# Kernel optimization log

Hardware: AMD Instinct MI355X
Metric: run time of the kernel (lower is better)

Reference implementation:

```python
import jax, jax.numpy as jnp
import numpy as np

B, N_PER_GRAPH = 16, 512          # uniform graphs -> to_dense_batch is a reshape
N_TOKENS = B * N_PER_GRAPH
M = 32                            # neighbors per node
D_MODEL, D_EDGE, H = 256, 128, 8


def _layernorm(x, g, b, eps=1e-5):
    m = jnp.mean(x, axis=-1, keepdims=True)
    v = jnp.mean((x - m) ** 2, axis=-1, keepdims=True)
    return (x - m) * jax.lax.rsqrt(v + eps) * g + b


def _frame_ops():
    # 2^3 = 8 sign-flip operations, matches FrameAveraging.create_ops
    d = jnp.array([-1.0, 1.0], dtype=jnp.float32)
    g = jnp.meshgrid(d, d, d, indexing='ij')
    return jnp.stack(g, axis=-1).reshape(8, 3)


def _forward(token_embs, geo_feats, edge_feats, neighbor_indices, neighbor_masks,
             ln_qkv_g, ln_qkv_b, W_qkv, b_qkv, ln_e_g, ln_e_b, W_qkv_e, b_qkv_e,
             w_attn, w_edge, W_gate, b_gate, W_fc1, b_fc1, ln_h_g, ln_h_b,
             W_fc2, b_fc2, W_fa, b_fa):
    n = token_embs.shape[0]
    d_head = D_MODEL // H
    de_head = D_EDGE // H
    # qkv transformation
    qkv = _layernorm(token_embs, ln_qkv_g, ln_qkv_b) @ W_qkv + b_qkv
    q, k, v = [a.reshape(n, H, d_head) for a in jnp.split(qkv, 3, axis=-1)]
    qkve = _layernorm(edge_feats, ln_e_g, ln_e_b) @ W_qkv_e + b_qkv_e
    qe, ve = [a.reshape(n, M, H, de_head) for a in jnp.split(qkve, 2, axis=-1)]
    gate = jax.nn.sigmoid(token_embs @ W_gate + b_gate)            # [n,1]
    # GAT-style MLP attention over gathered neighbors
    message = q[:, None] + k[neighbor_indices]                     # [n,M,H,d]
    attn = jnp.einsum('nmhd,d->nmh', message, w_attn) \
         + jnp.einsum('nmhe,e->nmh', qe, w_edge)
    attn = jnp.where(neighbor_masks[..., None], attn, -1e9)
    attn = jax.nn.softmax(jnp.transpose(attn, (0, 2, 1)), axis=-1)  # [n,H,M]
    # context aggregation
    v_n = v[neighbor_indices]                                      # [n,M,H,d]
    scalar_ctx = jnp.einsum('nhm,nmhd->nhd', attn, v_n).reshape(n, -1)
    edge_ctx = jnp.einsum('nhm,nmhd->nhd', attn, ve).reshape(n, -1)
    hcat = jnp.concatenate([scalar_ctx, edge_ctx], axis=-1)
    hmid = _layernorm(jax.nn.gelu(hcat @ W_fc1 + b_fc1, approximate=False), ln_h_g, ln_h_b)
    scalar_out = hmid @ W_fc2 + b_fc2 + token_embs
    # geometric branch with frame averaging (n_heads > 1 path)
    Xb = geo_feats.reshape(B, N_PER_GRAPH, 3)                      # dense batch, full mask
    center = Xb.mean(axis=1)                                       # [B,3]
    Xc = Xb - center[:, None]
    C = jax.lax.stop_gradient(jnp.einsum('bni,bnj->bij', Xc, Xc))  # backward=False -> detach
    _, V = jnp.linalg.eigh(C)                                      # symmetric, UPLO irrelevant
    ops = _frame_ops()
    F_ops = jax.lax.stop_gradient(ops[None, :, None, :] * V[:, None])  # [B,8,3,3]
    h_fr = jnp.einsum('bpj,boji->bopi', Xc, F_ops)                 # [B,8,N,3]
    geo_f = jnp.transpose(h_fr, (1, 0, 2, 3)).reshape(8, n, 3)     # frame-major, node order b*N+p
    geo_neigh = geo_f[:, neighbor_indices]                         # [8,n,M,3]
    geo_ctx = jnp.einsum('nhm,fnmd->fnhd', attn, geo_neigh)        # [8,n,H,3]
    agg = jax.nn.silu(jnp.einsum('fnhd,h->fnd', geo_ctx, W_fa) + b_fa)  # W_frame_agg
    geo_b = jnp.transpose(agg, (1, 0, 2)).reshape(B, N_PER_GRAPH, 8, 3)
    geo_b = jnp.transpose(geo_b, (0, 2, 1, 3))                     # [B,8,N,3]
    inv = jnp.einsum('boij,bopj->bopi', F_ops, geo_b).mean(axis=1) + center[:, None]
    geo_context = inv.reshape(n, 3)
    geo_out = geo_context * gate + geo_feats * (1.0 - gate)
    return scalar_out, geo_out


def setup_inputs() -> dict:
    key = jax.random.key(0)
    ks = jax.random.split(key, 16)
    r = lambda k, shape, s=0.02: (jax.random.normal(k, shape) * s).astype(jnp.float32)
    token_embs = jax.random.normal(ks[0], (N_TOKENS, D_MODEL), dtype=jnp.float32)
    geo_feats = jax.random.normal(ks[1], (N_TOKENS, 3), dtype=jnp.float32)
    edge_feats = jax.random.normal(ks[2], (N_TOKENS, M, D_EDGE), dtype=jnp.float32)
    base = (jnp.arange(N_TOKENS) // N_PER_GRAPH) * N_PER_GRAPH
    neighbor_indices = base[:, None] + jax.random.randint(ks[3], (N_TOKENS, M), 0, N_PER_GRAPH)
    batch_idx = jnp.arange(N_TOKENS) // N_PER_GRAPH
    neighbor_masks = jax.random.uniform(ks[4], (N_TOKENS, M)) < 0.9
    d_head, de_head = D_MODEL // H, D_EDGE // H
    return dict(
        token_embs=token_embs, geo_feats=geo_feats, edge_feats=edge_feats,
        neighbor_indices=neighbor_indices, batch_idx=batch_idx, neighbor_masks=neighbor_masks,
        ln_qkv_g=jnp.ones(D_MODEL), ln_qkv_b=jnp.zeros(D_MODEL),
        W_qkv=r(ks[5], (D_MODEL, 3 * D_MODEL)), b_qkv=jnp.zeros(3 * D_MODEL),
        ln_e_g=jnp.ones(D_EDGE), ln_e_b=jnp.zeros(D_EDGE),
        W_qkv_e=r(ks[6], (D_EDGE, 2 * D_EDGE)), b_qkv_e=jnp.zeros(2 * D_EDGE),
        w_attn=r(ks[7], (d_head,), 0.1), w_edge=r(ks[8], (de_head,), 0.1),
        W_gate=jnp.zeros((D_MODEL, 1)), b_gate=jnp.ones((1,)),   # _init_params
        W_fc1=r(ks[9], (D_MODEL + D_EDGE, D_MODEL)), b_fc1=jnp.zeros(D_MODEL),
        ln_h_g=jnp.ones(D_MODEL), ln_h_b=jnp.zeros(D_MODEL),
        W_fc2=r(ks[10], (D_MODEL, D_MODEL)), b_fc2=jnp.zeros(D_MODEL),
        W_fa=r(ks[11], (H,), 0.3), b_fa=jnp.zeros((1,)),
    )


def reference(token_embs, geo_feats, edge_feats, neighbor_indices, batch_idx, neighbor_masks,
              ln_qkv_g, ln_qkv_b, W_qkv, b_qkv, ln_e_g, ln_e_b, W_qkv_e, b_qkv_e,
              w_attn, w_edge, W_gate, b_gate, W_fc1, b_fc1, ln_h_g, ln_h_b,
              W_fc2, b_fc2, W_fa, b_fa):
    # batch_idx is uniform (arange // N_PER_GRAPH); dense batching handled by reshape
    return _forward(token_embs, geo_feats, edge_feats, neighbor_indices, neighbor_masks,
                    ln_qkv_g, ln_qkv_b, W_qkv, b_qkv, ln_e_g, ln_e_b, W_qkv_e, b_qkv_e,
                    w_attn, w_edge, W_gate, b_gate, W_fc1, b_fc1, ln_h_g, ln_h_b,
                    W_fc2, b_fc2, W_fa, b_fa)
```

## Files before the change

kernel.cpp:

```cpp
#include <hip/hip_runtime.h>
#include <math.h>

#define NTOK 8192
#define NPG  512
#define MNEI 32
#define DM   256
#define DE   128
#define NH   8

#define OFF_WV    0u
#define OFF_WQAK  65536u
#define OFF_BCAT  69632u
#define OFF_WEF   69904u
#define OFF_BEF   70928u
#define OFF_FLAG  70936u
#define OFF_QA    70944u
#define OFF_KA    136480u
#define OFF_GATE  202016u
#define OFF_VW    210208u
#define OFF_PROJ  2307360u
#define OFF_VMAT  2331936u
#define OFF_CEN   2332080u
#define OFF_HCAT  2332128u

#define OUT_GEO_OFF 2097152

__device__ __forceinline__ void fma4x4(const float4 a, const float4 w, float4* acc) {
    acc[0].x += a.x*w.x; acc[0].y += a.x*w.y; acc[0].z += a.x*w.z; acc[0].w += a.x*w.w;
    acc[1].x += a.y*w.x; acc[1].y += a.y*w.y; acc[1].z += a.y*w.z; acc[1].w += a.y*w.w;
    acc[2].x += a.z*w.x; acc[2].y += a.z*w.y; acc[2].z += a.z*w.z; acc[2].w += a.z*w.w;
    acc[3].x += a.w*w.x; acc[3].y += a.w*w.y; acc[3].z += a.w*w.z; acc[3].w += a.w*w.w;
}

__device__ __forceinline__ float dot4(const float4 a, const float4 b) {
    return a.x*b.x + a.y*b.y + a.z*b.z + a.w*b.w;
}

__global__ __launch_bounds__(256) void k_fold(
    const float* __restrict__ Wqkv, const float* __restrict__ bqkv,
    const float* __restrict__ Wqkve, const float* __restrict__ bqkve,
    const float* __restrict__ w_attn, const float* __restrict__ w_edge,
    const int* __restrict__ maskp, float* __restrict__ ws)
{
    int t = threadIdx.x;
    if (blockIdx.x == 0) {
        __shared__ int sbad, sflt;
        if (t == 0) { sbad = 0; sflt = 0; }
        __syncthreads();
        int bad = 0, flt = 0;
        for (int i = 0; i < 256; i++) {
            unsigned int w = (unsigned int)maskp[i*256 + t];
            if (w > 1u) bad = 1;
            if (w == 0x3F800000u) flt = 1;
        }
        if (bad) atomicOr(&sbad, 1);
        if (flt) atomicOr(&sflt, 1);
        __syncthreads();
        if (t == 0) {
            int f = sflt ? 2 : (sbad ? 1 : 0);
            ((int*)(ws + OFF_FLAG))[0] = f;
        }
        return;
    }
    int gid = (blockIdx.x - 1) * 256 + t;
    if (gid < 65536) {
        int k = gid >> 8, c = gid & 255;
        ws[OFF_WV + gid] = Wqkv[k*768 + 512 + c];
    } else if (gid < 69632) {
        int idx = gid - 65536;
        int c = idx >> 8, k = idx & 255;
        int h = c & 7; int off = (c < 8) ? 0 : 256;
        float s = 0.f;
        for (int d = 0; d < 32; d++) s += Wqkv[k*768 + off + h*32 + d] * w_attn[d];
        ws[OFF_WQAK + idx] = s;
    } else if (gid < 69632 + 272) {
        int c = gid - 69632;
        float val;
        if (c < 16) {
            int h = c & 7; int off = (c < 8) ? 0 : 256;
            float s = 0.f;
            for (int d = 0; d < 32; d++) s += bqkv[off + h*32 + d] * w_attn[d];
            val = s;
        } else {
            val = bqkv[512 + (c - 16)];
        }
        ws[OFF_BCAT + c] = val;
    } else if (gid < 69904 + 1024) {
        int i = gid - 69904;
        int h = i >> 7, r = i & 127;
        float s = 0.f;
        for (int e = 0; e < 16; e++) s += Wqkve[r*256 + h*16 + e] * w_edge[e];
        ws[OFF_WEF + i] = s;
    } else if (gid < 70928 + 8) {
        int h = gid - 70928;
        float s = 0.f;
        for (int e = 0; e < 16; e++) s += bqkve[h*16 + e] * w_edge[e];
        ws[OFF_BEF + h] = s;
    }
}

__global__ __launch_bounds__(256) void k_tokprep(
    const float* __restrict__ tok, const float* __restrict__ ln_g,
    const float* __restrict__ ln_b, const float* __restrict__ Wgate,
    const float* __restrict__ bgate, float* __restrict__ ws)
{
    __shared__ __align__(16) float sln[256 * 12];
    int t = threadIdx.x;
    int tok0 = blockIdx.x * 8;

    #pragma unroll
    for (int q = 0; q < 8; q++)
        sln[t*12 + q] = tok[(size_t)(tok0 + q) * 256 + t];
    __syncthreads();

    int wave = t >> 6, lane = t & 63;
    for (int rr = 0; rr < 2; rr++) {
        int tt = wave * 2 + rr;
        float s = 0.f, gdot = 0.f;
        float xs[4];
        #pragma unroll
        for (int q = 0; q < 4; q++) {
            int k = lane + 64*q;
            float x = sln[k*12 + tt];
            xs[q] = x; s += x; gdot += x * Wgate[k];
        }
        for (int m = 32; m >= 1; m >>= 1) { s += __shfl_xor(s,m,64); gdot += __shfl_xor(gdot,m,64); }
        float mu = s * (1.0f/256.0f);
        float vs = 0.f;
        #pragma unroll
        for (int q = 0; q < 4; q++) { float d = xs[q]-mu; vs += d*d; }
        for (int m = 32; m >= 1; m >>= 1) vs += __shfl_xor(vs,m,64);
        float rinv = rsqrtf(vs*(1.0f/256.0f)+1e-5f);
        #pragma unroll
        for (int q = 0; q < 4; q++) {
            int k = lane + 64*q;
            sln[k*12 + tt] = (xs[q]-mu)*rinv*ln_g[k] + ln_b[k];
        }
        if (lane == 0) ws[OFF_GATE + tok0 + tt] = 1.0f/(1.0f+expf(-(gdot + bgate[0])));
    }
    __syncthreads();

    if (t < 128) {
        int i = t >> 6, j = t & 63;
        const float* Wc = ws + OFF_WV + 4*j;
        float4 acc[4];
        acc[0] = acc[1] = acc[2] = acc[3] = make_float4(0.f,0.f,0.f,0.f);
        #pragma unroll 8
        for (int k = 0; k < 256; k++) {
            float4 a4 = *(const float4*)&sln[k*12 + 4*i];
            float4 w4 = *(const float4*)&Wc[(size_t)k*256];
            fma4x4(a4, w4, acc);
        }
        float4 b4 = *(const float4*)&ws[OFF_BCAT + 16 + 4*j];
        #pragma unroll
        for (int ti = 0; ti < 4; ti++) {
            int n = tok0 + 4*i + ti;
            float4 v = acc[ti];
            v.x += b4.x; v.y += b4.y; v.z += b4.z; v.w += b4.w;
            *(float4*)&ws[OFF_VW + (size_t)n*256 + 4*j] = v;
        }
    } else {
        int wave3 = (t >> 6) - 2;
        int col = t & 15, tp = (t & 63) >> 4;
        int tokn = wave3*4 + tp;
        const float* wq = ws + OFF_WQAK + col*256;
        float acc = 0.f;
        #pragma unroll 8
        for (int k4 = 0; k4 < 64; k4++) {
            float4 w4 = *(const float4*)&wq[4*k4];
            acc += w4.x * sln[(4*k4+0)*12 + tokn]
                 + w4.y * sln[(4*k4+1)*12 + tokn]
                 + w4.z * sln[(4*k4+2)*12 + tokn]
                 + w4.w * sln[(4*k4+3)*12 + tokn];
        }
        acc += ws[OFF_BCAT + col];
        int n = tok0 + tokn;
        if (col < 8) ws[OFF_QA + n*8 + col] = acc;
        else         ws[OFF_KA + n*8 + (col - 8)] = acc;
    }
}

__global__ __launch_bounds__(256) void k_geo(const float* __restrict__ geo, float* __restrict__ ws)
{
    __shared__ float sred[4 * 9];
    __shared__ float sres[9];
    __shared__ float sV[9];
    int t = threadIdx.x, g = blockIdx.x;
    int wave = t >> 6, lane = t & 63;
    const float* gp = geo + (size_t)g * NPG * 3;

    float x0[2], y0[2], z0[2];
    float sx = 0.f, sy = 0.f, sz = 0.f;
    for (int i = 0; i < 2; i++) {
        int p = t + 256 * i;
        x0[i] = gp[p*3 + 0]; y0[i] = gp[p*3 + 1]; z0[i] = gp[p*3 + 2];
        sx += x0[i]; sy += y0[i]; sz += z0[i];
    }
    {
        float vals[3] = {sx, sy, sz};
        for (int q = 0; q < 3; q++) {
            float v = vals[q];
            for (int m = 32; m >= 1; m >>= 1) v += __shfl_xor(v, m, 64);
            if (lane == 0) sred[wave*9 + q] = v;
        }
    }
    __syncthreads();
    if (t < 3) {
        float s = 0.f;
        for (int w = 0; w < 4; w++) s += sred[w*9 + t];
        sres[t] = s * (1.0f / 512.0f);
    }
    __syncthreads();
    float cx = sres[0], cy = sres[1], cz = sres[2];

    float c6[6] = {0.f, 0.f, 0.f, 0.f, 0.f, 0.f};
    for (int i = 0; i < 2; i++) {
        float dx = x0[i] - cx, dy = y0[i] - cy, dz = z0[i] - cz;
        c6[0] += dx*dx; c6[1] += dx*dy; c6[2] += dx*dz;
        c6[3] += dy*dy; c6[4] += dy*dz; c6[5] += dz*dz;
    }
    for (int q = 0; q < 6; q++) {
        float v = c6[q];
        for (int m = 32; m >= 1; m >>= 1) v += __shfl_xor(v, m, 64);
        if (lane == 0) sred[wave*9 + q] = v;
    }
    __syncthreads();
    if (t < 6) {
        float s = 0.f;
        for (int w = 0; w < 4; w++) s += sred[w*9 + t];
        sres[t] = s;
    }
    __syncthreads();

    if (t == 0) {
        double a[3][3];
        a[0][0] = sres[0]; a[0][1] = a[1][0] = sres[1]; a[0][2] = a[2][0] = sres[2];
        a[1][1] = sres[3]; a[1][2] = a[2][1] = sres[4]; a[2][2] = sres[5];
        double v[3][3] = {{1,0,0},{0,1,0},{0,0,1}};
        const int ps[3] = {0, 0, 1}, qs[3] = {1, 2, 2};
        for (int sweep = 0; sweep < 10; sweep++) {
            for (int pi = 0; pi < 3; pi++) {
                int p = ps[pi], q = qs[pi];
                double apq = a[p][q];
                if (fabs(apq) < 1e-300) continue;
                double theta = (a[q][q] - a[p][p]) / (2.0 * apq);
                double tt = ((theta >= 0.0) ? 1.0 : -1.0) / (fabs(theta) + sqrt(theta*theta + 1.0));
                double c = 1.0 / sqrt(tt*tt + 1.0), s = tt * c;
                int k = 3 - p - q;
                double app = a[p][p], aqq = a[q][q], akp = a[k][p], akq = a[k][q];
                a[p][p] = app - tt * apq;
                a[q][q] = aqq + tt * apq;
                a[p][q] = 0.0; a[q][p] = 0.0;
                a[k][p] = c*akp - s*akq; a[p][k] = a[k][p];
                a[k][q] = s*akp + c*akq; a[q][k] = a[k][q];
                for (int kk = 0; kk < 3; kk++) {
                    double vp = v[kk][p], vq = v[kk][q];
                    v[kk][p] = c*vp - s*vq;
                    v[kk][q] = s*vp + c*vq;
                }
            }
        }
        for (int r = 0; r < 3; r++)
            for (int c2 = 0; c2 < 3; c2++) {
                float fv = (float)v[r][c2];
                sV[r*3 + c2] = fv;
                ws[OFF_VMAT + g*9 + r*3 + c2] = fv;
            }
        ws[OFF_CEN + g*3 + 0] = cx;
        ws[OFF_CEN + g*3 + 1] = cy;
        ws[OFF_CEN + g*3 + 2] = cz;
    }
    __syncthreads();

    for (int i = 0; i < 2; i++) {
        int p = t + 256 * i;
        float dx = x0[i] - cx, dy = y0[i] - cy, dz = z0[i] - cz;
        for (int c = 0; c < 3; c++) {
            float pr = dx * sV[0*3 + c] + dy * sV[1*3 + c] + dz * sV[2*3 + c];
            ws[OFF_PROJ + (size_t)(g*NPG + p)*3 + c] = pr;
        }
    }
}

__global__ __launch_bounds__(256) void k_attn(
    const float* __restrict__ edge, const int* __restrict__ nbr,
    const void* __restrict__ maskp,
    const float* __restrict__ lneg, const float* __restrict__ lneb,
    const float* __restrict__ bqkve, const float* __restrict__ Wqkve,
    const float* __restrict__ Wfa, const float* __restrict__ bfa,
    const float* __restrict__ geo, float* __restrict__ ws, float* __restrict__ out)
{
    __shared__ __align__(16) float se[32 * 132];
    __shared__ __align__(16) float uSWE[8 * 132];
    __shared__ __align__(16) float sew[8 * 132];
    __shared__ __align__(16) float sattn[8 * 36];
    __shared__ int   snbr[32];
    __shared__ int   smask[32];
    __shared__ float sqa[8], sbef[8];
    __shared__ float sg3[4];

    int t = threadIdx.x;
    int n = blockIdx.x;
    int g = n >> 9;
    int flag = ((const int*)(ws + OFF_FLAG))[0];

    if (t < 32) {
        snbr[t] = nbr[n*32 + t];
        int mv;
        if (flag == 1)      mv = (int)((const unsigned char*)maskp)[n*32 + t];
        else if (flag == 2) mv = (((const float*)maskp)[n*32 + t] != 0.0f) ? 1 : 0;
        else                mv = ((const int*)maskp)[n*32 + t];
        smask[t] = mv;
    }
    if (t < 8) { sqa[t] = ws[OFF_QA + n*8 + t]; sbef[t] = ws[OFF_BEF + t]; }
    {
        int idx = t * 4;
        int h = idx >> 7, r = idx & 127;
        int sub = r >> 4, c = r & 15;
        *(float4*)&uSWE[sub*132 + h*16 + c] = *(const float4*)&ws[OFF_WEF + idx];
    }
    {
        const float4* ep = (const float4*)(edge + (size_t)n * 4096);
        #pragma unroll
        for (int j = 0; j < 4; j++) {
            int l = j*1024 + t*4;
            float4 v4 = ep[l >> 2];
            int m = l >> 7, r = l & 127;
            *(float4*)&se[m*132 + r] = v4;
        }
    }
    __syncthreads();

    int m = t >> 3, sub = t & 7;
    {
        int base = m*132 + sub*16;
        float4 x0 = *(float4*)&se[base + 0];
        float4 x1 = *(float4*)&se[base + 4];
        float4 x2 = *(float4*)&se[base + 8];
        float4 x3 = *(float4*)&se[base + 12];
        float s = x0.x+x0.y+x0.z+x0.w + x1.x+x1.y+x1.z+x1.w
                + x2.x+x2.y+x2.z+x2.w + x3.x+x3.y+x3.z+x3.w;
        for (int mm = 4; mm >= 1; mm >>= 1) s += __shfl_xor(s, mm, 8);
        float mu = s * (1.0f / 128.0f);
        float vs = (x0.x-mu)*(x0.x-mu) + (x0.y-mu)*(x0.y-mu) + (x0.z-mu)*(x0.z-mu) + (x0.w-mu)*(x0.w-mu)
                 + (x1.x-mu)*(x1.x-mu) + (x1.y-mu)*(x1.y-mu) + (x1.z-mu)*(x1.z-mu) + (x1.w-mu)*(x1.w-mu)
                 + (x2.x-mu)*(x2.x-mu) + (x2.y-mu)*(x2.y-mu) + (x2.z-mu)*(x2.z-mu) + (x2.w-mu)*(x2.w-mu)
                 + (x3.x-mu)*(x3.x-mu) + (x3.y-mu)*(x3.y-mu) + (x3.z-mu)*(x3.z-mu) + (x3.w-mu)*(x3.w-mu);
        for (int mm = 4; mm >= 1; mm >>= 1) vs += __shfl_xor(vs, mm, 8);
        float rinv = rsqrtf(vs * (1.0f / 128.0f) + 1e-5f);
        const float4* gp4 = (const float4*)(lneg + sub*16);
        const float4* bp4 = (const float4*)(lneb + sub*16);
        float4 g0 = gp4[0], g1 = gp4[1], g2 = gp4[2], g3 = gp4[3];
        float4 b0 = bp4[0], b1 = bp4[1], b2 = bp4[2], b3 = bp4[3];
        x0.x=(x0.x-mu)*rinv*g0.x+b0.x; x0.y=(x0.y-mu)*rinv*g0.y+b0.y;
        x0.z=(x0.z-mu)*rinv*g0.z+b0.z; x0.w=(x0.w-mu)*rinv*g0.w+b0.w;
        x1.x=(x1.x-mu)*rinv*g1.x+b1.x; x1.y=(x1.y-mu)*rinv*g1.y+b1.y;
        x1.z=(x1.z-mu)*rinv*g1.z+b1.z; x1.w=(x1.w-mu)*rinv*g1.w+b1.w;
        x2.x=(x2.x-mu)*rinv*g2.x+b2.x; x2.y=(x2.y-mu)*rinv*g2.y+b2.y;
        x2.z=(x2.z-mu)*rinv*g2.z+b2.z; x2.w=(x2.w-mu)*rinv*g2.w+b2.w;
        x3.x=(x3.x-mu)*rinv*g3.x+b3.x; x3.y=(x3.y-mu)*rinv*g3.y+b3.y;
        x3.z=(x3.z-mu)*rinv*g3.z+b3.z; x3.w=(x3.w-mu)*rinv*g3.w+b3.w;
        *(float4*)&se[base + 0]  = x0;
        *(float4*)&se[base + 4]  = x1;
        *(float4*)&se[base + 8]  = x2;
        *(float4*)&se[base + 12] = x3;

        float accl[8];
        const float* wb = &uSWE[sub*132];
        #pragma unroll
        for (int h = 0; h < 8; h++) {
            const float4* wp = (const float4*)(wb + h*16);
            accl[h] = dot4(x0,wp[0]) + dot4(x1,wp[1]) + dot4(x2,wp[2]) + dot4(x3,wp[3]);
        }
        #pragma unroll
        for (int st = 1; st < 8; st <<= 1) {
            #pragma unroll
            for (int h = 0; h < 8; h++) accl[h] += __shfl_xor(accl[h], st, 8);
        }
        float myacc = accl[0];
        #pragma unroll
        for (int h = 1; h < 8; h++) myacc = (sub == h) ? accl[h] : myacc;
        float lg = sqa[sub] + sbef[sub] + myacc + ws[OFF_KA + snbr[m]*8 + sub];
        if (!smask[m]) lg = -1e9f;
        sattn[sub*36 + m] = lg;
    }
    __syncthreads();

    {
        int h = t >> 5, m2 = t & 31;
        float x = sattn[h*36 + m2];
        float mx = x;
        for (int mm = 16; mm >= 1; mm >>= 1) mx = fmaxf(mx, __shfl_xor(mx, mm, 32));
        float e = expf(x - mx);
        float sum = e;
        for (int mm = 16; mm >= 1; mm >>= 1) sum += __shfl_xor(sum, mm, 32);
        sattn[h*36 + m2] = e / sum;
    }
    __syncthreads();

    float* sq = uSWE;

    float4 accS = make_float4(0.f,0.f,0.f,0.f);
    if (t < 128) {
        int half = t >> 6, c4 = t & 63;
        int h = c4 >> 3;
        const float* vw = ws + OFF_VW;
        #pragma unroll 4
        for (int mi = 0; mi < 16; mi++) {
            int mm2 = half*16 + mi;
            float a = sattn[h*36 + mm2];
            int row = snbr[mm2];
            float4 v4 = *(const float4*)&vw[(size_t)row*256 + 4*c4];
            accS.x += a*v4.x; accS.y += a*v4.y; accS.z += a*v4.z; accS.w += a*v4.w;
        }
        if (half) *(float4*)&sq[c4*4] = accS;
        if (t < 32) {
            float wmv = 0.f;
            #pragma unroll
            for (int h2 = 0; h2 < 8; h2++) wmv += Wfa[h2] * sattn[h2*36 + t];
            int row = snbr[t];
            const float* pp = ws + OFF_PROJ + (size_t)row*3;
            float q0 = wmv * pp[0], q1 = wmv * pp[1], q2 = wmv * pp[2];
            for (int st = 16; st >= 1; st >>= 1) {
                q0 += __shfl_xor(q0, st, 32);
                q1 += __shfl_xor(q1, st, 32);
                q2 += __shfl_xor(q2, st, 32);
            }
            if (t < 3) {
                float sd = (t == 0) ? q0 : (t == 1) ? q1 : q2;
                float bb = bfa[0];
                float p1 = sd + bb, p2 = -sd + bb;
                float s1v = p1 / (1.0f + expf(-p1));
                float s2v = p2 / (1.0f + expf(-p2));
                sg3[t] = 0.5f * (s1v - s2v);
            }
        }
    } else {
        int rq = t & 31, hb = (t >> 5) - 4;
        float4 e1 = make_float4(0.f,0.f,0.f,0.f);
        float4 e2 = make_float4(0.f,0.f,0.f,0.f);
        #pragma unroll
        for (int mq = 0; mq < 8; mq++) {
            float4 a4a = *(const float4*)&sattn[hb*36 + 4*mq];
            float4 a4b = *(const float4*)&sattn[(hb+4)*36 + 4*mq];
            float aa[4] = {a4a.x, a4a.y, a4a.z, a4a.w};
            float ab[4] = {a4b.x, a4b.y, a4b.z, a4b.w};
            #pragma unroll
            for (int c = 0; c < 4; c++) {
                int mm2 = 4*mq + c;
                float4 e4 = *(const float4*)&se[mm2*132 + rq*4];
                e1.x += aa[c]*e4.x; e1.y += aa[c]*e4.y; e1.z += aa[c]*e4.z; e1.w += aa[c]*e4.w;
                e2.x += ab[c]*e4.x; e2.y += ab[c]*e4.y; e2.z += ab[c]*e4.z; e2.w += ab[c]*e4.w;
            }
        }
        *(float4*)&sew[hb*132 + rq*4]     = e1;
        *(float4*)&sew[(hb+4)*132 + rq*4] = e2;
    }
    __syncthreads();

    float* sec = se;
    float4 accE = make_float4(0.f,0.f,0.f,0.f);
    {
        int col4 = t & 31, rgrp = t >> 5;
        int h2 = col4 >> 2;
        const float* wqb = Wqkve + 128 + 4*col4;
        #pragma unroll 4
        for (int ri = 0; ri < 16; ri++) {
            int r = rgrp*16 + ri;
            float sv = sew[h2*132 + r];
            float4 w4 = *(const float4*)&wqb[(size_t)r*256];
            accE.x += sv*w4.x; accE.y += sv*w4.y; accE.z += sv*w4.z; accE.w += sv*w4.w;
        }
        if (t < 64) {
            float4 p = *(const float4*)&sq[t*4];
            float4 tot;
            tot.x = accS.x + p.x; tot.y = accS.y + p.y;
            tot.z = accS.z + p.z; tot.w = accS.w + p.w;
            *(float4*)&ws[OFF_HCAT + (size_t)n*384 + 4*t] = tot;
        }
        *(float4*)&sec[rgrp*128 + col4*4] = accE;
    }
    __syncthreads();

    if (t < 128) {
        float ec = bqkve[128 + t];
        #pragma unroll
        for (int g2 = 0; g2 < 8; g2++) ec += sec[g2*128 + t];
        ws[OFF_HCAT + (size_t)n*384 + 256 + t] = ec;
    }
    if (t < 3) {
        const float* Vm = ws + OFF_VMAT + g*9;
        float gc = Vm[t*3+0]*sg3[0] + Vm[t*3+1]*sg3[1] + Vm[t*3+2]*sg3[2] + ws[OFF_CEN + g*3 + t];
        float gt = ws[OFF_GATE + n];
        out[OUT_GEO_OFF + (size_t)n*3 + t] = gc * gt + geo[(size_t)n*3 + t] * (1.0f - gt);
    }
}

__global__ __launch_bounds__(256) void k_mlp(
    const float* __restrict__ tok, const float* __restrict__ Wfc1,
    const float* __restrict__ bfc1, const float* __restrict__ lnhg,
    const float* __restrict__ lnhb, const float* __restrict__ Wfc2,
    const float* __restrict__ bfc2, const float* __restrict__ ws,
    float* __restrict__ out)
{
    __shared__ __align__(16) float A[384 * 12];
    __shared__ __align__(16) float R[128 * 16];
    int t = threadIdx.x;
    int tok0 = blockIdx.x * 8;
    int i2 = (t >> 6) & 1, kh = t >> 7, j = t & 63;
    const float* hc = ws + OFF_HCAT;

    #pragma unroll
    for (int q = 0; q < 12; q++) {
        int idx = q*256 + t;
        int tt = idx / 384;
        int k  = idx - tt*384;
        A[k*12 + tt] = hc[(size_t)tok0*384 + idx];
    }
    __syncthreads();

    float4 acc1[4];
    acc1[0] = acc1[1] = acc1[2] = acc1[3] = make_float4(0.f,0.f,0.f,0.f);
    {
        const float* wp = Wfc1 + 4*j;
        int kbase = kh * 192;
        #pragma unroll 8
        for (int kk = 0; kk < 192; kk++) {
            int k = kbase + kk;
            float4 a4 = *(const float4*)&A[k*12 + 4*i2];
            float4 w4 = *(const float4*)&wp[(size_t)k*256];
            fma4x4(a4, w4, acc1);
        }
    }
    if (kh == 1) {
        int rowid = t - 128;
        #pragma unroll
        for (int ti = 0; ti < 4; ti++) *(float4*)&R[rowid*16 + ti*4] = acc1[ti];
    }
    __syncthreads();

    float h[4][4];
    if (kh == 0) {
        float4 b4 = *(const float4*)&bfc1[4*j];
        #pragma unroll
        for (int ti = 0; ti < 4; ti++) {
            float4 p = *(const float4*)&R[t*16 + ti*4];
            float xv[4] = {acc1[ti].x + p.x + b4.x, acc1[ti].y + p.y + b4.y,
                           acc1[ti].z + p.z + b4.z, acc1[ti].w + p.w + b4.w};
            #pragma unroll
            for (int c = 0; c < 4; c++) {
                float x = xv[c];
                h[ti][c] = 0.5f * x * (1.0f + erff(x * 0.70710678118654752f));
            }
        }
        float s[4], qv[4];
        #pragma unroll
        for (int ti = 0; ti < 4; ti++) {
            s[ti]  = h[ti][0] + h[ti][1] + h[ti][2] + h[ti][3];
            qv[ti] = h[ti][0]*h[ti][0] + h[ti][1]*h[ti][1] + h[ti][2]*h[ti][2] + h[ti][3]*h[ti][3];
        }
        for (int m = 32; m >= 1; m >>= 1)
            #pragma unroll
            for (int ti = 0; ti < 4; ti++) {
                s[ti]  += __shfl_xor(s[ti], m, 64);
                qv[ti] += __shfl_xor(qv[ti], m, 64);
            }
        float4 g4 = *(const float4*)&lnhg[4*j];
        float4 b42 = *(const float4*)&lnhb[4*j];
        float gg[4] = {g4.x, g4.y, g4.z, g4.w};
        float bb[4] = {b42.x, b42.y, b42.z, b42.w};
        #pragma unroll
        for (int ti = 0; ti < 4; ti++) {
            float mu = s[ti] * (1.0f/256.0f);
            float var = qv[ti] * (1.0f/256.0f) - mu*mu;
            float rinv = rsqrtf(var + 1e-5f);
            #pragma unroll
            for (int c = 0; c < 4; c++) {
                float hn = (h[ti][c] - mu) * rinv * gg[c] + bb[c];
                A[(4*j + c)*12 + 4*i2 + ti] = hn;
            }
        }
    }
    __syncthreads();

    float4 acc2[4];
    acc2[0] = acc2[1] = acc2[2] = acc2[3] = make_float4(0.f,0.f,0.f,0.f);
    {
        const float* wp = Wfc2 + 4*j;
        int kbase = kh * 128;
        #pragma unroll 8
        for (int kk = 0; kk < 128; kk++) {
            int k = kbase + kk;
            float4 a4 = *(const float4*)&A[k*12 + 4*i2];
            float4 w4 = *(const float4*)&wp[(size_t)k*256];
            fma4x4(a4, w4, acc2);
        }
    }
    if (kh == 1) {
        int rowid = t - 128;
        #pragma unroll
        for (int ti = 0; ti < 4; ti++) *(float4*)&R[rowid*16 + ti*4] = acc2[ti];
    }
    __syncthreads();

    if (kh == 0) {
        float4 b4 = *(const float4*)&bfc2[4*j];
        #pragma unroll
        for (int ti = 0; ti < 4; ti++) {
            float4 p = *(const float4*)&R[t*16 + ti*4];
            size_t o = (size_t)(tok0 + 4*i2 + ti) * 256 + 4*j;
            float4 r4 = *(const float4*)&tok[o];
            float4 v;
            v.x = acc2[ti].x + p.x + b4.x + r4.x;
            v.y = acc2[ti].y + p.y + b4.y + r4.y;
            v.z = acc2[ti].z + p.z + b4.z + r4.z;
            v.w = acc2[ti].w + p.w + b4.w + r4.w;
            *(float4*)&out[o] = v;
        }
    }
}

extern "C" void kernel_launch(void* const* d_in, const int* in_sizes, int n_in,
                              void* d_out, int out_size, void* d_ws, size_t ws_size,
                              hipStream_t stream) {
    (void)in_sizes; (void)n_in; (void)out_size; (void)ws_size;
    const float* tok   = (const float*)d_in[0];
    const float* geo   = (const float*)d_in[1];
    const float* edge  = (const float*)d_in[2];
    const int*   nbr   = (const int*)d_in[3];
    const void*  maskp = d_in[5];
    const float* ln_qkv_g = (const float*)d_in[6];
    const float* ln_qkv_b = (const float*)d_in[7];
    const float* Wqkv  = (const float*)d_in[8];
    const float* bqkv  = (const float*)d_in[9];
    const float* ln_e_g = (const float*)d_in[10];
    const float* ln_e_b = (const float*)d_in[11];
    const float* Wqkve = (const float*)d_in[12];
    const float* bqkve = (const float*)d_in[13];
    const float* w_attn = (const float*)d_in[14];
    const float* w_edge = (const float*)d_in[15];
    const float* Wgate = (const float*)d_in[16];
    const float* bgate = (const float*)d_in[17];
    const float* Wfc1  = (const float*)d_in[18];
    const float* bfc1  = (const float*)d_in[19];
    const float* lnhg  = (const float*)d_in[20];
    const float* lnhb  = (const float*)d_in[21];
    const float* Wfc2  = (const float*)d_in[22];
    const float* bfc2  = (const float*)d_in[23];
    const float* Wfa   = (const float*)d_in[24];
    const float* bfa   = (const float*)d_in[25];
    float* ws  = (float*)d_ws;
    float* out = (float*)d_out;

    k_fold<<<dim3(279), dim3(256), 0, stream>>>(Wqkv, bqkv, Wqkve, bqkve, w_attn, w_edge,
                                                (const int*)maskp, ws);
    k_tokprep<<<dim3(1024), dim3(256), 0, stream>>>(tok, ln_qkv_g, ln_qkv_b, Wgate, bgate, ws);
    k_geo<<<dim3(16), dim3(256), 0, stream>>>(geo, ws);
    k_attn<<<dim3(8192), dim3(256), 0, stream>>>(edge, nbr, maskp, ln_e_g, ln_e_b, bqkve,
                                                 Wqkve, Wfa, bfa, geo, ws, out);
    k_mlp<<<dim3(1024), dim3(256), 0, stream>>>(tok, Wfc1, bfc1, lnhg, lnhb, Wfc2, bfc2, ws, out);
}
```

Before: 401.6 us.

## Fold edge LayerNorm affine into weights and defer normalization scaling in attention kernel

Folds the edge LayerNorm gain into the precomputed edge-attention weights and the LN bias into the per-head query bias, so the attention kernel only centers the edge rows and applies rinv afterward. Edge rows are loaded straight into registers instead of staging through shared memory first, which removes one barrier and the gamma/beta loads per element. The LN affine is instead applied after the attention-weighted edge sum. Work is also reorganised per wave so wave 0 does the full 32-neighbor value gather, and mask reads move inline. This trades a small extra fold cost and changed floating-point rounding order for less per-token arithmetic and shared-memory traffic.

```diff
diff --git a/kernel.cpp b/kernel.cpp
--- a/kernel.cpp
+++ b/kernel.cpp
@@ -40,6 +40,7 @@
     const float* __restrict__ Wqkv, const float* __restrict__ bqkv,
     const float* __restrict__ Wqkve, const float* __restrict__ bqkve,
     const float* __restrict__ w_attn, const float* __restrict__ w_edge,
+    const float* __restrict__ lneg, const float* __restrict__ lneb,
     const int* __restrict__ maskp, float* __restrict__ ws)
 {
     int t = threadIdx.x;
@@ -76,10 +77,21 @@
     } else if (gid < 69632 + 272) {
         int c = gid - 69632;
         float val;
-        if (c < 16) {
-            int h = c & 7; int off = (c < 8) ? 0 : 256;
+        if (c < 8) {
+            int h = c;
             float s = 0.f;
-            for (int d = 0; d < 32; d++) s += bqkv[off + h*32 + d] * w_attn[d];
+            for (int d = 0; d < 32; d++) s += bqkv[h*32 + d] * w_attn[d];
+            for (int e = 0; e < 16; e++) s += bqkve[h*16 + e] * w_edge[e];
+            for (int r = 0; r < 128; r++) {
+                float wef = 0.f;
+                for (int e = 0; e < 16; e++) wef += Wqkve[r*256 + h*16 + e] * w_edge[e];
+                s += lneb[r] * wef;
+            }
+            val = s;
+        } else if (c < 16) {
+            int h = c & 7;
+            float s = 0.f;
+            for (int d = 0; d < 32; d++) s += bqkv[256 + h*32 + d] * w_attn[d];
             val = s;
         } else {
             val = bqkv[512 + (c - 16)];
@@ -90,12 +102,7 @@
         int h = i >> 7, r = i & 127;
         float s = 0.f;
         for (int e = 0; e < 16; e++) s += Wqkve[r*256 + h*16 + e] * w_edge[e];
-        ws[OFF_WEF + i] = s;
-    } else if (gid < 70928 + 8) {
-        int h = gid - 70928;
-        float s = 0.f;
-        for (int e = 0; e < 16; e++) s += bqkve[h*16 + e] * w_edge[e];
-        ws[OFF_BEF + h] = s;
+        ws[OFF_WEF + i] = s * lneg[r];
     }
 }
 
@@ -292,11 +299,9 @@
 {
     __shared__ __align__(16) float se[32 * 132];
     __shared__ __align__(16) float uSWE[8 * 132];
-    __shared__ __align__(16) float sew[8 * 132];
     __shared__ __align__(16) float sattn[8 * 36];
+    __shared__ float srinv[32];
     __shared__ int   snbr[32];
-    __shared__ int   smask[32];
-    __shared__ float sqa[8], sbef[8];
     __shared__ float sg3[4];
 
     int t = threadIdx.x;
@@ -304,66 +309,34 @@
     int g = n >> 9;
     int flag = ((const int*)(ws + OFF_FLAG))[0];
 
-    if (t < 32) {
-        snbr[t] = nbr[n*32 + t];
-        int mv;
-        if (flag == 1)      mv = (int)((const unsigned char*)maskp)[n*32 + t];
-        else if (flag == 2) mv = (((const float*)maskp)[n*32 + t] != 0.0f) ? 1 : 0;
-        else                mv = ((const int*)maskp)[n*32 + t];
-        smask[t] = mv;
-    }
-    if (t < 8) { sqa[t] = ws[OFF_QA + n*8 + t]; sbef[t] = ws[OFF_BEF + t]; }
+    int m = t >> 3, sub = t & 7;
+
+    const float4* xp = (const float4*)(edge + (size_t)n * 4096 + m*128 + sub*16);
+    float4 x0 = xp[0], x1 = xp[1], x2 = xp[2], x3 = xp[3];
     {
         int idx = t * 4;
         int h = idx >> 7, r = idx & 127;
-        int sub = r >> 4, c = r & 15;
-        *(float4*)&uSWE[sub*132 + h*16 + c] = *(const float4*)&ws[OFF_WEF + idx];
-    }
+        int s2 = r >> 4, c = r & 15;
+        *(float4*)&uSWE[s2*132 + h*16 + c] = *(const float4*)&ws[OFF_WEF + idx];
+    }
+    if (t < 32) snbr[t] = nbr[n*32 + t];
+    __syncthreads();
+
     {
-        const float4* ep = (const float4*)(edge + (size_t)n * 4096);
-        #pragma unroll
-        for (int j = 0; j < 4; j++) {
-            int l = j*1024 + t*4;
-            float4 v4 = ep[l >> 2];
-            int m = l >> 7, r = l & 127;
-            *(float4*)&se[m*132 + r] = v4;
-        }
-    }
-    __syncthreads();
-
-    int m = t >> 3, sub = t & 7;
-    {
-        int base = m*132 + sub*16;
-        float4 x0 = *(float4*)&se[base + 0];
-        float4 x1 = *(float4*)&se[base + 4];
-        float4 x2 = *(float4*)&se[base + 8];
-        float4 x3 = *(float4*)&se[base + 12];
         float s = x0.x+x0.y+x0.z+x0.w + x1.x+x1.y+x1.z+x1.w
                 + x2.x+x2.y+x2.z+x2.w + x3.x+x3.y+x3.z+x3.w;
         for (int mm = 4; mm >= 1; mm >>= 1) s += __shfl_xor(s, mm, 8);
         float mu = s * (1.0f / 128.0f);
-        float vs = (x0.x-mu)*(x0.x-mu) + (x0.y-mu)*(x0.y-mu) + (x0.z-mu)*(x0.z-mu) + (x0.w-mu)*(x0.w-mu)
-                 + (x1.x-mu)*(x1.x-mu) + (x1.y-mu)*(x1.y-mu) + (x1.z-mu)*(x1.z-mu) + (x1.w-mu)*(x1.w-mu)
-                 + (x2.x-mu)*(x2.x-mu) + (x2.y-mu)*(x2.y-mu) + (x2.z-mu)*(x2.z-mu) + (x2.w-mu)*(x2.w-mu)
-                 + (x3.x-mu)*(x3.x-mu) + (x3.y-mu)*(x3.y-mu) + (x3.z-mu)*(x3.z-mu) + (x3.w-mu)*(x3.w-mu);
+        x0.x-=mu; x0.y-=mu; x0.z-=mu; x0.w-=mu;
+        x1.x-=mu; x1.y-=mu; x1.z-=mu; x1.w-=mu;
+        x2.x-=mu; x2.y-=mu; x2.z-=mu; x2.w-=mu;
+        x3.x-=mu; x3.y-=mu; x3.z-=mu; x3.w-=mu;
+        float vs = dot4(x0,x0) + dot4(x1,x1) + dot4(x2,x2) + dot4(x3,x3);
         for (int mm = 4; mm >= 1; mm >>= 1) vs += __shfl_xor(vs, mm, 8);
         float rinv = rsqrtf(vs * (1.0f / 128.0f) + 1e-5f);
-        const float4* gp4 = (const float4*)(lneg + sub*16);
-        const float4* bp4 = (const float4*)(lneb + sub*16);
-        float4 g0 = gp4[0], g1 = gp4[1], g2 = gp4[2], g3 = gp4[3];
-        float4 b0 = bp4[0], b1 = bp4[1], b2 = bp4[2], b3 = bp4[3];
-        x0.x=(x0.x-mu)*rinv*g0.x+b0.x; x0.y=(x0.y-mu)*rinv*g0.y+b0.y;
-        x0.z=(x0.z-mu)*rinv*g0.z+b0.z; x0.w=(x0.w-mu)*rinv*g0.w+b0.w;
-        x1.x=(x1.x-mu)*rinv*g1.x+b1.x; x1.y=(x1.y-mu)*rinv*g1.y+b1.y;
-        x1.z=(x1.z-mu)*rinv*g1.z+b1.z; x1.w=(x1.w-mu)*rinv*g1.w+b1.w;
-        x2.x=(x2.x-mu)*rinv*g2.x+b2.x; x2.y=(x2.y-mu)*rinv*g2.y+b2.y;
-        x2.z=(x2.z-mu)*rinv*g2.z+b2.z; x2.w=(x2.w-mu)*rinv*g2.w+b2.w;
-        x3.x=(x3.x-mu)*rinv*g3.x+b3.x; x3.y=(x3.y-mu)*rinv*g3.y+b3.y;
-        x3.z=(x3.z-mu)*rinv*g3.z+b3.z; x3.w=(x3.w-mu)*rinv*g3.w+b3.w;
-        *(float4*)&se[base + 0]  = x0;
-        *(float4*)&se[base + 4]  = x1;
-        *(float4*)&se[base + 8]  = x2;
-        *(float4*)&se[base + 12] = x3;
+        float4* sp = (float4*)&se[m*132 + sub*16];
+        sp[0] = x0; sp[1] = x1; sp[2] = x2; sp[3] = x3;
+        if (sub == 0) srinv[m] = rinv;
 
         float accl[8];
         const float* wb = &uSWE[sub*132];
@@ -380,8 +353,16 @@
         float myacc = accl[0];
         #pragma unroll
         for (int h = 1; h < 8; h++) myacc = (sub == h) ? accl[h] : myacc;
-        float lg = sqa[sub] + sbef[sub] + myacc + ws[OFF_KA + snbr[m]*8 + sub];
-        if (!smask[m]) lg = -1e9f;
+
+        int mv;
+        if (flag == 1)      mv = (int)((const unsigned char*)maskp)[n*32 + m];
+        else if (flag == 2) mv = (((const float*)maskp)[n*32 + m] != 0.0f) ? 1 : 0;
+        else                mv = ((const int*)maskp)[n*32 + m];
+
+        float lg = myacc * rinv
+                 + ws[OFF_QA + n*8 + sub]
+                 + ws[OFF_KA + (size_t)snbr[m]*8 + sub];
+        if (!mv) lg = -1e9f;
         sattn[sub*36 + m] = lg;
     }
     __syncthreads();
@@ -398,27 +379,28 @@
     }
     __syncthreads();
 
-    float* sq = uSWE;
-
-    float4 accS = make_float4(0.f,0.f,0.f,0.f);
-    if (t < 128) {
-        int half = t >> 6, c4 = t & 63;
-        int h = c4 >> 3;
+    float* sew = uSWE;
+
+    int wave = t >> 6;
+    if (wave == 0) {
+        int c4 = t, h = c4 >> 3;
         const float* vw = ws + OFF_VW;
+        float4 acc = make_float4(0.f,0.f,0.f,0.f);
         #pragma unroll 4
-        for (int mi = 0; mi < 16; mi++) {
-            int mm2 = half*16 + mi;
-            float a = sattn[h*36 + mm2];
-            int row = snbr[mm2];
+        for (int mi = 0; mi < 32; mi++) {
+            float a = sattn[h*36 + mi];
+            int row = snbr[mi];
             float4 v4 = *(const float4*)&vw[(size_t)row*256 + 4*c4];
-            accS.x += a*v4.x; accS.y += a*v4.y; accS.z += a*v4.z; accS.w += a*v4.w;
-        }
-        if (half) *(float4*)&sq[c4*4] = accS;
-        if (t < 32) {
+            acc.x += a*v4.x; acc.y += a*v4.y; acc.z += a*v4.z; acc.w += a*v4.w;
+        }
+        *(float4*)&ws[OFF_HCAT + (size_t)n*384 + 4*c4] = acc;
+    } else if (wave == 1) {
+        int lm = t - 64;
+        if (lm < 32) {
             float wmv = 0.f;
             #pragma unroll
-            for (int h2 = 0; h2 < 8; h2++) wmv += Wfa[h2] * sattn[h2*36 + t];
-            int row = snbr[t];
+            for (int h2 = 0; h2 < 8; h2++) wmv += Wfa[h2] * sattn[h2*36 + lm];
+            int row = snbr[lm];
             const float* pp = ws + OFF_PROJ + (size_t)row*3;
             float q0 = wmv * pp[0], q1 = wmv * pp[1], q2 = wmv * pp[2];
             for (int st = 16; st >= 1; st >>= 1) {
@@ -426,44 +408,46 @@
                 q1 += __shfl_xor(q1, st, 32);
                 q2 += __shfl_xor(q2, st, 32);
             }
-            if (t < 3) {
-                float sd = (t == 0) ? q0 : (t == 1) ? q1 : q2;
+            if (lm < 3) {
+                float sd = (lm == 0) ? q0 : (lm == 1) ? q1 : q2;
                 float bb = bfa[0];
                 float p1 = sd + bb, p2 = -sd + bb;
                 float s1v = p1 / (1.0f + expf(-p1));
                 float s2v = p2 / (1.0f + expf(-p2));
-                sg3[t] = 0.5f * (s1v - s2v);
+                sg3[lm] = 0.5f * (s1v - s2v);
             }
         }
     } else {
-        int rq = t & 31, hb = (t >> 5) - 4;
+        int rq = t & 31, hb = (t >> 5) & 3;
         float4 e1 = make_float4(0.f,0.f,0.f,0.f);
         float4 e2 = make_float4(0.f,0.f,0.f,0.f);
-        #pragma unroll
-        for (int mq = 0; mq < 8; mq++) {
-            float4 a4a = *(const float4*)&sattn[hb*36 + 4*mq];
-            float4 a4b = *(const float4*)&sattn[(hb+4)*36 + 4*mq];
-            float aa[4] = {a4a.x, a4a.y, a4a.z, a4a.w};
-            float ab[4] = {a4b.x, a4b.y, a4b.z, a4b.w};
-            #pragma unroll
-            for (int c = 0; c < 4; c++) {
-                int mm2 = 4*mq + c;
-                float4 e4 = *(const float4*)&se[mm2*132 + rq*4];
-                e1.x += aa[c]*e4.x; e1.y += aa[c]*e4.y; e1.z += aa[c]*e4.z; e1.w += aa[c]*e4.w;
-                e2.x += ab[c]*e4.x; e2.y += ab[c]*e4.y; e2.z += ab[c]*e4.z; e2.w += ab[c]*e4.w;
-            }
-        }
-        *(float4*)&sew[hb*132 + rq*4]     = e1;
-        *(float4*)&sew[(hb+4)*132 + rq*4] = e2;
+        #pragma unroll 4
+        for (int mi = 0; mi < 32; mi++) {
+            float ri = srinv[mi];
+            float a1 = sattn[hb*36 + mi] * ri;
+            float a2 = sattn[(hb+4)*36 + mi] * ri;
+            float4 x4 = *(const float4*)&se[mi*132 + 4*rq];
+            e1.x += a1*x4.x; e1.y += a1*x4.y; e1.z += a1*x4.z; e1.w += a1*x4.w;
+            e2.x += a2*x4.x; e2.y += a2*x4.y; e2.z += a2*x4.z; e2.w += a2*x4.w;
+        }
+        float4 g4 = *(const float4*)&lneg[4*rq];
+        float4 b4 = *(const float4*)&lneb[4*rq];
+        float4 o1, o2;
+        o1.x = g4.x*e1.x + b4.x; o1.y = g4.y*e1.y + b4.y;
+        o1.z = g4.z*e1.z + b4.z; o1.w = g4.w*e1.w + b4.w;
+        o2.x = g4.x*e2.x + b4.x; o2.y = g4.y*e2.y + b4.y;
+        o2.z = g4.z*e2.z + b4.z; o2.w = g4.w*e2.w + b4.w;
+        *(float4*)&sew[hb*132 + 4*rq]     = o1;
+        *(float4*)&sew[(hb+4)*132 + 4*rq] = o2;
     }
     __syncthreads();
 
     float* sec = se;
-    float4 accE = make_float4(0.f,0.f,0.f,0.f);
     {
         int col4 = t & 31, rgrp = t >> 5;
         int h2 = col4 >> 2;
         const float* wqb = Wqkve + 128 + 4*col4;
+        float4 accE = make_float4(0.f,0.f,0.f,0.f);
         #pragma unroll 4
         for (int ri = 0; ri < 16; ri++) {
             int r = rgrp*16 + ri;
@@ -471,14 +455,7 @@
             float4 w4 = *(const float4*)&wqb[(size_t)r*256];
             accE.x += sv*w4.x; accE.y += sv*w4.y; accE.z += sv*w4.z; accE.w += sv*w4.w;
         }
-        if (t < 64) {
-            float4 p = *(const float4*)&sq[t*4];
-            float4 tot;
-            tot.x = accS.x + p.x; tot.y = accS.y + p.y;
-            tot.z = accS.z + p.z; tot.w = accS.w + p.w;
-            *(float4*)&ws[OFF_HCAT + (size_t)n*384 + 4*t] = tot;
-        }
-        *(float4*)&sec[rgrp*128 + col4*4] = accE;
+        *(float4*)&sec[rgrp*128 + 4*col4] = accE;
     }
     __syncthreads();
 
@@ -653,7 +630,7 @@
     float* out = (float*)d_out;
 
     k_fold<<<dim3(279), dim3(256), 0, stream>>>(Wqkv, bqkv, Wqkve, bqkve, w_attn, w_edge,
-                                                (const int*)maskp, ws);
+                                                ln_e_g, ln_e_b, (const int*)maskp, ws);
     k_tokprep<<<dim3(1024), dim3(256), 0, stream>>>(tok, ln_qkv_g, ln_qkv_b, Wgate, bgate, ws);
     k_geo<<<dim3(16), dim3(256), 0, stream>>>(geo, ws);
     k_attn<<<dim3(8192), dim3(256), 0, stream>>>(edge, nbr, maskp, ln_e_g, ln_e_b, bqkve,
```

Result: faster. 393.3 us (-2.1%).
